# Optimization experiments

Hardware: AMD Instinct MI355X
Metric: run time of the kernel (lower is better)

Reference implementation:

```python
import jax, jax.numpy as jnp
import numpy as np

B, N, J, D = 16384, 4096, 256, 9  # batch, input_dim, output_dim, ultimate_depth


def _rotate(state, angle):
    # state: [J, N], angle: [J]
    # Circulant gate: out[i] = cos*v[i] - sin*v[(i+1)%N] + sin*v[(i-1)%N]
    c = jnp.cos(angle)[:, None]
    s = jnp.sin(angle)[:, None]
    return c * state - s * jnp.roll(state, -1, axis=1) + s * jnp.roll(state, 1, axis=1)


def setup_inputs() -> dict:
    key = jax.random.key(0)
    k0, k1, k2, k3 = jax.random.split(key, 4)
    return {
        "x": jax.random.normal(k0, (B, N), dtype=jnp.float32),
        "ultimate_weights": jax.random.normal(k1, (D, N, J), dtype=jnp.float32),
        "classical_weights": jax.random.normal(k2, (N, J), dtype=jnp.float32),
        "classical_biases": jax.random.normal(k3, (J,), dtype=jnp.float32),
    }


def reference(x, ultimate_weights, classical_weights, classical_biases):
    batch = x.shape[0]
    depth, n_in, _ = ultimate_weights.shape
    n_out = classical_weights.shape[1]

    classical = x @ classical_weights + classical_biases  # [B, J]

    # Ultimate processing: batch-independent; vectorized over output dim j.
    state = jnp.ones((n_out, n_in), dtype=x.dtype) / jnp.sqrt(
        jnp.asarray(n_in, dtype=x.dtype)
    )  # [J, N]
    angles = ultimate_weights[:, :n_out, :3]  # [D, J, 3]

    def step(st, ang):  # ang: [J, 3] -> consciousness, intelligence, wisdom gates
        st = _rotate(st, ang[:, 0])
        st = _rotate(st, ang[:, 1])
        st = _rotate(st, ang[:, 2])
        return st, None

    state, _ = jax.lax.scan(step, state, angles)
    prob = jnp.abs(state[:, 0]) ** 2  # [J]
    ultimate = jnp.broadcast_to(prob, (batch, n_out))

    return jnp.tanh(classical + ultimate)
```

## Files before the change

### kernel.cpp

```cpp
#include <hip/hip_runtime.h>
#include <math.h>

#define K_DIM 4096
#define N_DIM 256
#define M_DIM 16384
#define BK 32
#define NSTAGES (K_DIM / BK)
#define BUF_BYTES 24576

typedef short bf8v __attribute__((ext_vector_type(8)));
typedef float f4v __attribute__((ext_vector_type(4)));
typedef unsigned short us8 __attribute__((ext_vector_type(8)));

union FragU { unsigned u[4]; bf8v v; };

__device__ __forceinline__ void gl_lds16(const void* g, void* l) {
    __builtin_amdgcn_global_load_lds(
        (const __attribute__((address_space(1))) unsigned int*)g,
        (__attribute__((address_space(3))) unsigned int*)l, 16, 0, 0);
}

__global__ void split_w_kernel(const float* __restrict__ W,
                               unsigned short* __restrict__ Whi,
                               unsigned short* __restrict__ Wlo) {
    __shared__ float tile[32][132];
    const int s = blockIdx.x;
    const int nblk = blockIdx.y;
    const int t = threadIdx.x;
    #pragma unroll
    for (int i = 0; i < 4; ++i) {
        int flat = i * 1024 + t * 4;
        int k = flat >> 7;
        int n = flat & 127;
        *(float4*)&tile[k][n] =
            *(const float4*)&W[(size_t)(s * 32 + k) * N_DIM + nblk * 128 + n];
    }
    __syncthreads();
    #pragma unroll
    for (int i = 0; i < 2; ++i) {
        int g = i * 256 + t;
        int kpart = g >> 7;
        int nrow = g & 127;
        unsigned short h8[8], l8[8];
        #pragma unroll
        for (int j = 0; j < 8; ++j) {
            float f = tile[kpart * 8 + j][nrow];
            unsigned u = __float_as_uint(f);
            unsigned hh = u + 0x7fffu + ((u >> 16) & 1u);
            float r = f - __uint_as_float(hh & 0xffff0000u);
            h8[j] = (unsigned short)(hh >> 16);
            l8[j] = (unsigned short)(__float_as_uint(r) >> 16);
        }
        size_t o = ((size_t)(nblk * NSTAGES + s) * 512 + g) * 8;
        *(us8*)&Whi[o] = *(us8*)&h8[0];
        *(us8*)&Wlo[o] = *(us8*)&l8[0];
    }
}

__global__ void beta_kernel(const float* __restrict__ uw,
                            const float* __restrict__ bias,
                            float* __restrict__ beta) {
    int j = threadIdx.x;
    float p = 1.0f / 4096.0f;
    #pragma unroll
    for (int d = 0; d < 9; ++d) {
        const float* a = uw + (size_t)d * (K_DIM * N_DIM) + (size_t)j * N_DIM;
        #pragma unroll
        for (int k = 0; k < 3; ++k) {
            float c = cosf(a[k]);
            p *= c * c;
        }
    }
    beta[j] = bias[j] + p;
}

__device__ __forceinline__ void cvt8(float4 f0, float4 f1, FragU& hi, FragU& lo) {
    float f[8] = {f0.x, f0.y, f0.z, f0.w, f1.x, f1.y, f1.z, f1.w};
    #pragma unroll
    for (int i = 0; i < 4; ++i) {
        float x0 = f[2 * i], x1 = f[2 * i + 1];
        unsigned u0 = __float_as_uint(x0), u1 = __float_as_uint(x1);
        unsigned h0 = u0 + 0x7fffu + ((u0 >> 16) & 1u);
        unsigned h1 = u1 + 0x7fffu + ((u1 >> 16) & 1u);
        hi.u[i] = (h0 >> 16) | (h1 & 0xffff0000u);
        float r0 = x0 - __uint_as_float(h0 & 0xffff0000u);
        float r1 = x1 - __uint_as_float(h1 & 0xffff0000u);
        lo.u[i] = (__float_as_uint(r0) >> 16) | (__float_as_uint(r1) & 0xffff0000u);
    }
}

__device__ __forceinline__ f4v mfma_bf16(bf8v a, bf8v b, f4v c) {
    return __builtin_amdgcn_mfma_f32_16x16x32_bf16(a, b, c, 0, 0, 0);
}

__device__ __forceinline__ void stage_tile(const float* gA0, const float* gA1,
                                           const unsigned short* gBh,
                                           const unsigned short* gBl,
                                           char* buf, int t, int s) {
    gl_lds16(gA0 + (size_t)s * BK, buf + t * 16);
    gl_lds16(gA1 + (size_t)s * BK, buf + (t + 256) * 16);
    const unsigned short* bh = gBh + (size_t)s * 4096;
    const unsigned short* bl = gBl + (size_t)s * 4096;
    gl_lds16(bh,        buf + 8192  + t * 16);
    gl_lds16(bh + 2048, buf + 8192  + (t + 256) * 16);
    gl_lds16(bl,        buf + 16384 + t * 16);
    gl_lds16(bl + 2048, buf + 16384 + (t + 256) * 16);
}

__global__ __launch_bounds__(256, 2)
void gemm_tanh_kernel(const float* __restrict__ X,
                      const unsigned short* __restrict__ Whi,
                      const unsigned short* __restrict__ Wlo,
                      const float* __restrict__ beta,
                      float* __restrict__ out) {
    __shared__ __align__(16) char lds[3 * BUF_BYTES];

    const int t = threadIdx.x;
    const int nblk = blockIdx.x;
    const int n0 = nblk * 128;
    const int m0 = blockIdx.y * 64;

    const int lane = t & 63;
    const int wave = t >> 6;
    const int wm = wave & 1;
    const int wn = wave >> 1;
    const int r16 = lane & 15;
    const int quad = lane >> 4;

    const float* gA0;
    const float* gA1;
    {
        int s0 = t, s1 = t + 256;
        int mr0 = s0 >> 3, kh0 = (s0 & 7) ^ (mr0 & 7);
        int mr1 = s1 >> 3, kh1 = (s1 & 7) ^ (mr1 & 7);
        gA0 = X + (size_t)(m0 + mr0) * K_DIM + kh0 * 4;
        gA1 = X + (size_t)(m0 + mr1) * K_DIM + kh1 * 4;
    }
    const unsigned short* gBh = Whi + (size_t)nblk * NSTAGES * 4096 + t * 8;
    const unsigned short* gBl = Wlo + (size_t)nblk * NSTAGES * 4096 + t * 8;

    f4v acc[2][4];
    #pragma unroll
    for (int mt = 0; mt < 2; ++mt)
        #pragma unroll
        for (int nt = 0; nt < 4; ++nt)
            acc[mt][nt] = (f4v)(0.0f);

    char* b0 = lds;
    char* b1 = lds + BUF_BYTES;
    char* b2 = lds + 2 * BUF_BYTES;

    stage_tile(gA0, gA1, gBh, gBl, b0, t, 0);
    stage_tile(gA0, gA1, gBh, gBl, b1, t, 1);

    for (int s = 0; s < NSTAGES; ++s) {
        if (s < NSTAGES - 2) {
            asm volatile("s_waitcnt vmcnt(6)\n\ts_barrier" ::: "memory");
            stage_tile(gA0, gA1, gBh, gBl, b2, t, s + 2);
        } else {
            asm volatile("s_waitcnt vmcnt(0)\n\ts_barrier" ::: "memory");
        }

        FragU ah[2], al[2];
        #pragma unroll
        for (int mt = 0; mt < 2; ++mt) {
            int mrow = wm * 32 + mt * 16 + r16;
            int khs0 = (quad * 2)     ^ (mrow & 7);
            int khs1 = (quad * 2 + 1) ^ (mrow & 7);
            float4 f0 = *(const float4*)(b0 + (mrow * 8 + khs0) * 16);
            float4 f1 = *(const float4*)(b0 + (mrow * 8 + khs1) * 16);
            cvt8(f0, f1, ah[mt], al[mt]);
        }
        FragU bh[4], bl[4];
        #pragma unroll
        for (int nt = 0; nt < 4; ++nt) {
            int nrow = wn * 64 + nt * 16 + r16;
            bh[nt].v = *(const bf8v*)(b0 + 8192  + (quad * 128 + nrow) * 16);
            bl[nt].v = *(const bf8v*)(b0 + 16384 + (quad * 128 + nrow) * 16);
        }
        #pragma unroll
        for (int nt = 0; nt < 4; ++nt) {
            acc[0][nt] = mfma_bf16(ah[0].v, bh[nt].v, acc[0][nt]);
            acc[0][nt] = mfma_bf16(al[0].v, bh[nt].v, acc[0][nt]);
            acc[0][nt] = mfma_bf16(ah[0].v, bl[nt].v, acc[0][nt]);
            acc[1][nt] = mfma_bf16(ah[1].v, bh[nt].v, acc[1][nt]);
            acc[1][nt] = mfma_bf16(al[1].v, bh[nt].v, acc[1][nt]);
            acc[1][nt] = mfma_bf16(ah[1].v, bl[nt].v, acc[1][nt]);
        }

        char* tmp = b0; b0 = b1; b1 = b2; b2 = tmp;
    }

    const int nbase = n0 + wn * 64;
    float bet[4];
    #pragma unroll
    for (int nt = 0; nt < 4; ++nt) bet[nt] = beta[nbase + nt * 16 + r16];

    const int mbase = m0 + wm * 32;
    #pragma unroll
    for (int mt = 0; mt < 2; ++mt) {
        #pragma unroll
        for (int nt = 0; nt < 4; ++nt) {
            const int col = nbase + nt * 16 + r16;
            #pragma unroll
            for (int r = 0; r < 4; ++r) {
                const int row = mbase + mt * 16 + quad * 4 + r;
                out[(size_t)row * N_DIM + col] = tanhf(acc[mt][nt][r] + bet[nt]);
            }
        }
    }
}

extern "C" void kernel_launch(void* const* d_in, const int* in_sizes, int n_in,
                              void* d_out, int out_size, void* d_ws, size_t ws_size,
                              hipStream_t stream) {
    const float* x    = (const float*)d_in[0];
    const float* uw   = (const float*)d_in[1];
    const float* W    = (const float*)d_in[2];
    const float* bias = (const float*)d_in[3];
    float* out = (float*)d_out;

    char* ws = (char*)d_ws;
    unsigned short* whi = (unsigned short*)(ws);
    unsigned short* wlo = (unsigned short*)(ws + (size_t)2 * 1024 * 1024);
    float* beta = (float*)(ws + (size_t)4 * 1024 * 1024);

    split_w_kernel<<<dim3(NSTAGES, N_DIM / 128), 256, 0, stream>>>(W, whi, wlo);
    beta_kernel<<<1, 256, 0, stream>>>(uw, bias, beta);

    dim3 grid(N_DIM / 128, M_DIM / 64);
    gemm_tanh_kernel<<<grid, 256, 0, stream>>>(x, whi, wlo, beta, out);
}
```

Before: 498.2 us.

## Restructure GEMM to full-N blocks with register-resident B and 32x32 MFMA

Each workgroup now covers 32 rows of M and all 256 output columns, with 8 waves each owning a 32-column slice. B fragments are pre-tiled into MFMA register layout and loaded straight from global into registers, so only the split A tile goes through a small double-buffered LDS. A is converted once per block with v_cvt_pk_bf16_f32 before the LDS write, not on every fragment read, and the MFMA shape moves to 32x32x16. This removes A reloads across the two N-blocks and the redundant per-wave conversion, at the cost of a very small M tile, B being streamed from L2 by every block, and a tight one-barrier-per-stage pipeline.

```diff
diff --git a/kernel.cpp b/kernel.cpp
--- a/kernel.cpp
+++ b/kernel.cpp
@@ -4,57 +4,19 @@
 #define K_DIM 4096
 #define N_DIM 256
 #define M_DIM 16384
-#define BK 32
-#define NSTAGES (K_DIM / BK)
-#define BUF_BYTES 24576
+#define NSTAGES 128
+#define ABUF 4096
 
 typedef short bf8v __attribute__((ext_vector_type(8)));
-typedef float f4v __attribute__((ext_vector_type(4)));
+typedef float f32x16 __attribute__((ext_vector_type(16)));
 typedef unsigned short us8 __attribute__((ext_vector_type(8)));
 
-union FragU { unsigned u[4]; bf8v v; };
+union AB { unsigned u[4]; bf8v v; };
 
-__device__ __forceinline__ void gl_lds16(const void* g, void* l) {
-    __builtin_amdgcn_global_load_lds(
-        (const __attribute__((address_space(1))) unsigned int*)g,
-        (__attribute__((address_space(3))) unsigned int*)l, 16, 0, 0);
-}
-
-__global__ void split_w_kernel(const float* __restrict__ W,
-                               unsigned short* __restrict__ Whi,
-                               unsigned short* __restrict__ Wlo) {
-    __shared__ float tile[32][132];
-    const int s = blockIdx.x;
-    const int nblk = blockIdx.y;
-    const int t = threadIdx.x;
-    #pragma unroll
-    for (int i = 0; i < 4; ++i) {
-        int flat = i * 1024 + t * 4;
-        int k = flat >> 7;
-        int n = flat & 127;
-        *(float4*)&tile[k][n] =
-            *(const float4*)&W[(size_t)(s * 32 + k) * N_DIM + nblk * 128 + n];
-    }
-    __syncthreads();
-    #pragma unroll
-    for (int i = 0; i < 2; ++i) {
-        int g = i * 256 + t;
-        int kpart = g >> 7;
-        int nrow = g & 127;
-        unsigned short h8[8], l8[8];
-        #pragma unroll
-        for (int j = 0; j < 8; ++j) {
-            float f = tile[kpart * 8 + j][nrow];
-            unsigned u = __float_as_uint(f);
-            unsigned hh = u + 0x7fffu + ((u >> 16) & 1u);
-            float r = f - __uint_as_float(hh & 0xffff0000u);
-            h8[j] = (unsigned short)(hh >> 16);
-            l8[j] = (unsigned short)(__float_as_uint(r) >> 16);
-        }
-        size_t o = ((size_t)(nblk * NSTAGES + s) * 512 + g) * 8;
-        *(us8*)&Whi[o] = *(us8*)&h8[0];
-        *(us8*)&Wlo[o] = *(us8*)&l8[0];
-    }
+__device__ __forceinline__ unsigned cvt_pk(float a, float b) {
+    unsigned r;
+    asm("v_cvt_pk_bf16_f32 %0, %1, %2" : "=v"(r) : "v"(a), "v"(b));
+    return r;
 }
 
 __global__ void beta_kernel(const float* __restrict__ uw,
@@ -74,140 +36,129 @@
     beta[j] = bias[j] + p;
 }
 
-__device__ __forceinline__ void cvt8(float4 f0, float4 f1, FragU& hi, FragU& lo) {
-    float f[8] = {f0.x, f0.y, f0.z, f0.w, f1.x, f1.y, f1.z, f1.w};
+__global__ void pretile_w_kernel(const float* __restrict__ W,
+                                 unsigned short* __restrict__ Bt) {
+    const int s = blockIdx.x;
+    const int t = threadIdx.x;
     #pragma unroll
-    for (int i = 0; i < 4; ++i) {
-        float x0 = f[2 * i], x1 = f[2 * i + 1];
-        unsigned u0 = __float_as_uint(x0), u1 = __float_as_uint(x1);
-        unsigned h0 = u0 + 0x7fffu + ((u0 >> 16) & 1u);
-        unsigned h1 = u1 + 0x7fffu + ((u1 >> 16) & 1u);
-        hi.u[i] = (h0 >> 16) | (h1 & 0xffff0000u);
-        float r0 = x0 - __uint_as_float(h0 & 0xffff0000u);
-        float r1 = x1 - __uint_as_float(h1 & 0xffff0000u);
-        lo.u[i] = (__float_as_uint(r0) >> 16) | (__float_as_uint(r1) & 0xffff0000u);
+    for (int g = 0; g < 8; ++g) {
+        const int G  = g * 256 + t;
+        const int w  = G >> 8;
+        const int h  = (G >> 7) & 1;
+        const int ks = (G >> 6) & 1;
+        const int l  = G & 63;
+        const int n  = w * 32 + (l & 31);
+        const int k0 = s * 32 + ks * 16 + (l >> 5) * 8;
+        unsigned short o8[8];
+        #pragma unroll
+        for (int j = 0; j < 8; ++j) {
+            float f = W[(size_t)(k0 + j) * N_DIM + n];
+            unsigned u = __float_as_uint(f);
+            unsigned hh = u + 0x7fffu + ((u >> 16) & 1u);
+            if (h == 0) {
+                o8[j] = (unsigned short)(hh >> 16);
+            } else {
+                float r = f - __uint_as_float(hh & 0xffff0000u);
+                unsigned ur = __float_as_uint(r);
+                o8[j] = (unsigned short)((ur + 0x7fffu + ((ur >> 16) & 1u)) >> 16);
+            }
+        }
+        *(us8*)&Bt[((size_t)s * 2048 + G) * 8] = *(us8*)&o8[0];
     }
 }
 
-__device__ __forceinline__ f4v mfma_bf16(bf8v a, bf8v b, f4v c) {
-    return __builtin_amdgcn_mfma_f32_16x16x32_bf16(a, b, c, 0, 0, 0);
+__global__ __launch_bounds__(512, 4)
+void gemm_tanh_kernel(const float* __restrict__ X,
+                      const unsigned short* __restrict__ Bt,
+                      const float* __restrict__ beta,
+                      float* __restrict__ out) {
+    __shared__ __align__(16) char lds[2 * ABUF];
+
+    const int t = threadIdx.x;
+    const int lane = t & 63;
+    const int w = t >> 6;
+    const int l31 = lane & 31;
+    const int lh = lane >> 5;
+    const int m0 = blockIdx.x * 32;
+
+    const int srow = t >> 4;
+    const int kp = t & 15;
+    const float* pa = X + (size_t)(m0 + srow) * K_DIM + kp * 2;
+    const int whi_off = srow * 128 + ((((kp >> 2)    ) ^ (srow & 7)) << 4) + (kp & 3) * 4;
+    const int wlo_off = srow * 128 + ((((kp >> 2) + 4) ^ (srow & 7)) << 4) + (kp & 3) * 4;
+
+    const int fx = (l31 & 7) << 4;
+    const int rb = l31 * 128;
+    const int ro_h0 = rb + (((0 + lh) << 4) ^ fx);
+    const int ro_h1 = rb + (((2 + lh) << 4) ^ fx);
+    const int ro_l0 = rb + (((4 + lh) << 4) ^ fx);
+    const int ro_l1 = rb + (((6 + lh) << 4) ^ fx);
+
+    const unsigned short* pb = Bt + w * 2048 + lane * 8;
+
+    f32x16 acc = (f32x16)(0.0f);
+    float2 araw;
+    AB bA[4], bB[4];
+
+#define LOADB(dst, sidx) { \
+    const unsigned short* p_ = pb + (size_t)(sidx) * 16384; \
+    dst[0].v = *(const bf8v*)(p_);           \
+    dst[1].v = *(const bf8v*)(p_ + 512);     \
+    dst[2].v = *(const bf8v*)(p_ + 1024);    \
+    dst[3].v = *(const bf8v*)(p_ + 1536); }
+
+#define CVTWR(ar, NB) { \
+    unsigned hp_ = cvt_pk(ar.x, ar.y); \
+    float r0_ = ar.x - __uint_as_float(hp_ << 16);           \
+    float r1_ = ar.y - __uint_as_float(hp_ & 0xffff0000u); \
+    unsigned lp_ = cvt_pk(r0_, r1_); \
+    *(unsigned*)(lds + (NB) + whi_off) = hp_; \
+    *(unsigned*)(lds + (NB) + wlo_off) = lp_; }
+
+#define MFMA(a, b) acc = __builtin_amdgcn_mfma_f32_32x32x16_bf16((a), (b), acc, 0, 0, 0)
+
+    {
+        float2 a0 = *(const float2*)pa;
+        CVTWR(a0, 0);
+        araw = *(const float2*)(pa + 32);
+        LOADB(bA, 0);
+        asm volatile("s_waitcnt lgkmcnt(0)\n\ts_barrier" ::: "memory");
+    }
+
+#define BODY(s, CB, NB, BCUR, BNXT) { \
+    CVTWR(araw, NB); \
+    araw = *(const float2*)(pa + (size_t)(((s) + 2) & 127) * 32); \
+    LOADB(BNXT, ((s) + 1) & 127); \
+    AB ah0, ah1, al0, al1; \
+    ah0.v = *(const bf8v*)(lds + (CB) + ro_h0); \
+    ah1.v = *(const bf8v*)(lds + (CB) + ro_h1); \
+    al0.v = *(const bf8v*)(lds + (CB) + ro_l0); \
+    al1.v = *(const bf8v*)(lds + (CB) + ro_l1); \
+    MFMA(ah0.v, BCUR[0].v); \
+    MFMA(al0.v, BCUR[0].v); \
+    MFMA(ah0.v, BCUR[2].v); \
+    MFMA(ah1.v, BCUR[1].v); \
+    MFMA(al1.v, BCUR[1].v); \
+    MFMA(ah1.v, BCUR[3].v); \
+    asm volatile("s_waitcnt lgkmcnt(0)\n\ts_barrier" ::: "memory"); \
 }
 
-__device__ __forceinline__ void stage_tile(const float* gA0, const float* gA1,
-                                           const unsigned short* gBh,
-                                           const unsigned short* gBl,
-                                           char* buf, int t, int s) {
-    gl_lds16(gA0 + (size_t)s * BK, buf + t * 16);
-    gl_lds16(gA1 + (size_t)s * BK, buf + (t + 256) * 16);
-    const unsigned short* bh = gBh + (size_t)s * 4096;
-    const unsigned short* bl = gBl + (size_t)s * 4096;
-    gl_lds16(bh,        buf + 8192  + t * 16);
-    gl_lds16(bh + 2048, buf + 8192  + (t + 256) * 16);
-    gl_lds16(bl,        buf + 16384 + t * 16);
-    gl_lds16(bl + 2048, buf + 16384 + (t + 256) * 16);
-}
-
-__global__ __launch_bounds__(256, 2)
-void gemm_tanh_kernel(const float* __restrict__ X,
-                      const unsigned short* __restrict__ Whi,
-                      const unsigned short* __restrict__ Wlo,
-                      const float* __restrict__ beta,
-                      float* __restrict__ out) {
-    __shared__ __align__(16) char lds[3 * BUF_BYTES];
-
-    const int t = threadIdx.x;
-    const int nblk = blockIdx.x;
-    const int n0 = nblk * 128;
-    const int m0 = blockIdx.y * 64;
-
-    const int lane = t & 63;
-    const int wave = t >> 6;
-    const int wm = wave & 1;
-    const int wn = wave >> 1;
-    const int r16 = lane & 15;
-    const int quad = lane >> 4;
-
-    const float* gA0;
-    const float* gA1;
-    {
-        int s0 = t, s1 = t + 256;
-        int mr0 = s0 >> 3, kh0 = (s0 & 7) ^ (mr0 & 7);
-        int mr1 = s1 >> 3, kh1 = (s1 & 7) ^ (mr1 & 7);
-        gA0 = X + (size_t)(m0 + mr0) * K_DIM + kh0 * 4;
-        gA1 = X + (size_t)(m0 + mr1) * K_DIM + kh1 * 4;
-    }
-    const unsigned short* gBh = Whi + (size_t)nblk * NSTAGES * 4096 + t * 8;
-    const unsigned short* gBl = Wlo + (size_t)nblk * NSTAGES * 4096 + t * 8;
-
-    f4v acc[2][4];
-    #pragma unroll
-    for (int mt = 0; mt < 2; ++mt)
-        #pragma unroll
-        for (int nt = 0; nt < 4; ++nt)
-            acc[mt][nt] = (f4v)(0.0f);
-
-    char* b0 = lds;
-    char* b1 = lds + BUF_BYTES;
-    char* b2 = lds + 2 * BUF_BYTES;
-
-    stage_tile(gA0, gA1, gBh, gBl, b0, t, 0);
-    stage_tile(gA0, gA1, gBh, gBl, b1, t, 1);
-
-    for (int s = 0; s < NSTAGES; ++s) {
-        if (s < NSTAGES - 2) {
-            asm volatile("s_waitcnt vmcnt(6)\n\ts_barrier" ::: "memory");
-            stage_tile(gA0, gA1, gBh, gBl, b2, t, s + 2);
-        } else {
-            asm volatile("s_waitcnt vmcnt(0)\n\ts_barrier" ::: "memory");
-        }
-
-        FragU ah[2], al[2];
-        #pragma unroll
-        for (int mt = 0; mt < 2; ++mt) {
-            int mrow = wm * 32 + mt * 16 + r16;
-            int khs0 = (quad * 2)     ^ (mrow & 7);
-            int khs1 = (quad * 2 + 1) ^ (mrow & 7);
-            float4 f0 = *(const float4*)(b0 + (mrow * 8 + khs0) * 16);
-            float4 f1 = *(const float4*)(b0 + (mrow * 8 + khs1) * 16);
-            cvt8(f0, f1, ah[mt], al[mt]);
-        }
-        FragU bh[4], bl[4];
-        #pragma unroll
-        for (int nt = 0; nt < 4; ++nt) {
-            int nrow = wn * 64 + nt * 16 + r16;
-            bh[nt].v = *(const bf8v*)(b0 + 8192  + (quad * 128 + nrow) * 16);
-            bl[nt].v = *(const bf8v*)(b0 + 16384 + (quad * 128 + nrow) * 16);
-        }
-        #pragma unroll
-        for (int nt = 0; nt < 4; ++nt) {
-            acc[0][nt] = mfma_bf16(ah[0].v, bh[nt].v, acc[0][nt]);
-            acc[0][nt] = mfma_bf16(al[0].v, bh[nt].v, acc[0][nt]);
-            acc[0][nt] = mfma_bf16(ah[0].v, bl[nt].v, acc[0][nt]);
-            acc[1][nt] = mfma_bf16(ah[1].v, bh[nt].v, acc[1][nt]);
-            acc[1][nt] = mfma_bf16(al[1].v, bh[nt].v, acc[1][nt]);
-            acc[1][nt] = mfma_bf16(ah[1].v, bl[nt].v, acc[1][nt]);
-        }
-
-        char* tmp = b0; b0 = b1; b1 = b2; b2 = tmp;
+    for (int s = 0; s < NSTAGES; s += 2) {
+        BODY(s,     0,    ABUF, bA, bB);
+        BODY(s + 1, ABUF, 0,    bB, bA);
     }
 
-    const int nbase = n0 + wn * 64;
-    float bet[4];
+#undef BODY
+#undef MFMA
+#undef CVTWR
+#undef LOADB
+
+    const float bet = beta[w * 32 + l31];
+    float* po = out + (size_t)(m0 + 4 * lh) * N_DIM + w * 32 + l31;
     #pragma unroll
-    for (int nt = 0; nt < 4; ++nt) bet[nt] = beta[nbase + nt * 16 + r16];
-
-    const int mbase = m0 + wm * 32;
-    #pragma unroll
-    for (int mt = 0; mt < 2; ++mt) {
-        #pragma unroll
-        for (int nt = 0; nt < 4; ++nt) {
-            const int col = nbase + nt * 16 + r16;
-            #pragma unroll
-            for (int r = 0; r < 4; ++r) {
-                const int row = mbase + mt * 16 + quad * 4 + r;
-                out[(size_t)row * N_DIM + col] = tanhf(acc[mt][nt][r] + bet[nt]);
-            }
-        }
+    for (int r = 0; r < 16; ++r) {
+        const int row = (r & 3) + 8 * (r >> 2);
+        po[(size_t)row * N_DIM] = tanhf(acc[r] + bet);
     }
 }
 
@@ -221,13 +172,11 @@
     float* out = (float*)d_out;
 
     char* ws = (char*)d_ws;
-    unsigned short* whi = (unsigned short*)(ws);
-    unsigned short* wlo = (unsigned short*)(ws + (size_t)2 * 1024 * 1024);
+    unsigned short* bt = (unsigned short*)ws;
     float* beta = (float*)(ws + (size_t)4 * 1024 * 1024);
 
-    split_w_kernel<<<dim3(NSTAGES, N_DIM / 128), 256, 0, stream>>>(W, whi, wlo);
+    pretile_w_kernel<<<dim3(NSTAGES), 256, 0, stream>>>(W, bt);
     beta_kernel<<<1, 256, 0, stream>>>(uw, bias, beta);
 
-    dim3 grid(N_DIM / 128, M_DIM / 64);
-    gemm_tanh_kernel<<<grid, 256, 0, stream>>>(x, whi, wlo, beta, out);
+    gemm_tanh_kernel<<<dim3(M_DIM / 32), 512, 0, stream>>>(x, bt, beta, out);
 }
```

After: 540.0 us. 1.08x slower.
